# Kernel tuning notes

Hardware: AMD Instinct MI355X
Metric: run time of the kernel (lower is better)

Reference implementation:

```python
import jax, jax.numpy as jnp
import numpy as np

EPS = 1e-5
MAX_NORM = 1.0 - 1e-5  # clamp for atanh / ball projection


def mob_add(u, v):
    # Mobius addition on each d_ball (last dim), c=1
    uv = jnp.sum(u * v, axis=-1, keepdims=True)
    uu = jnp.sum(u * u, axis=-1, keepdims=True)
    vv = jnp.sum(v * v, axis=-1, keepdims=True)
    num = (1.0 + 2.0 * uv + vv) * u + (1.0 - uu) * v
    den = 1.0 + 2.0 * uv + uu * vv
    return num / jnp.maximum(den, EPS)


def log_map_zero(y):
    # log map at origin, per ball (last dim)
    n = jnp.linalg.norm(y, axis=-1, keepdims=True)
    n_c = jnp.clip(n, EPS, MAX_NORM)
    return jnp.arctanh(n_c) * y / n_c


def mob_mat_mul_d(W, x, d):
    # W: (n_in, d, n_out, d); x: (B, n_in, d) -> (B, n_out, d)
    # Mobius matvec on the flattened product-ball representation.
    B = x.shape[0]
    x_f = x.reshape(B, -1)                      # (B, n_in*d)
    W_f = W.reshape(x_f.shape[-1], -1)          # (n_in*d, n_out*d)
    Mx = x_f @ W_f                              # (B, n_out*d)
    x_n = jnp.clip(jnp.linalg.norm(x_f, axis=-1, keepdims=True), EPS, MAX_NORM)
    Mx_n = jnp.maximum(jnp.linalg.norm(Mx, axis=-1, keepdims=True), EPS)
    res = jnp.tanh(Mx_n / x_n * jnp.arctanh(x_n)) * (Mx / Mx_n)
    return res.reshape(B, -1, d)


def mob_pointwise_prod(x, u):
    # diagonal Mobius scaling of hyperbolic x by euclidean gate u, per ball
    ux = u * x
    x_n = jnp.clip(jnp.linalg.norm(x, axis=-1, keepdims=True), EPS, MAX_NORM)
    ux_n = jnp.maximum(jnp.linalg.norm(ux, axis=-1, keepdims=True), EPS)
    return jnp.tanh(ux_n / x_n * jnp.arctanh(x_n)) * (ux / ux_n)


def transition(W, h, U, x, b, d):
    Wh = mob_mat_mul_d(W, h, d)
    Ux = mob_mat_mul_d(U, x, d)
    return mob_add(mob_add(Wh, Ux), b)


def setup_inputs() -> dict:
    key = jax.random.key(0)
    ks = jax.random.split(key, 8)
    B, I, H, D = 16384, 256, 256, 4
    k = (1.0 / H) ** 0.5
    # scale points to lie strictly inside the Poincare ball
    hyp_x = 0.02 * jax.random.normal(ks[0], (B, I, D), dtype=jnp.float32)
    hidden = 0.02 * jax.random.normal(ks[1], (B, H, D), dtype=jnp.float32)
    mk = lambda kk, n_in: jax.random.uniform(kk, (n_in, D, H, D), minval=-k, maxval=k, dtype=jnp.float32)
    return dict(
        hyp_x=hyp_x, hidden=hidden,
        w_z=mk(ks[2], H), w_r=mk(ks[3], H), w_h=mk(ks[4], H),
        u_z=mk(ks[5], I), u_r=mk(ks[6], I), u_h=mk(ks[7], I),
        b_z=jnp.zeros((H, D), jnp.float32),
        b_r=jnp.zeros((H, D), jnp.float32),
        b_h=jnp.zeros((H, D), jnp.float32),
    )


def reference(hyp_x, hidden, w_z, w_r, w_h, u_z, u_r, u_h, b_z, b_r, b_h):
    d = hyp_x.shape[-1]
    z = jax.nn.sigmoid(log_map_zero(transition(w_z, hidden, u_z, hyp_x, b_z, d)))
    r = jax.nn.sigmoid(log_map_zero(transition(w_r, hidden, u_r, hyp_x, b_r, d)))
    r_point_h = mob_pointwise_prod(hidden, r)
    # NOTE: original code uses u_r here (not u_h) -- kept faithful
    h_tilde = transition(w_h, r_point_h, u_r, hyp_x, b_h, d)
    minus_h_oplus_htilde = mob_add(-hidden, h_tilde)
    new_h = mob_add(hidden, mob_pointwise_prod(minus_h_oplus_htilde, z))
    return new_h
```

## Files before the change

### kernel.cpp

```cpp
#include <hip/hip_runtime.h>
#include <stdint.h>

#define EPSF 1e-5f
#define MAXNF (1.0f - 1e-5f)

typedef __attribute__((ext_vector_type(8))) short short8;
typedef __attribute__((ext_vector_type(4))) float floatx4;

__device__ __forceinline__ unsigned short f2bf(float f){
  union { float f; uint32_t u; } v; v.f = f;
  return (unsigned short)((v.u + 0x7FFFu + ((v.u >> 16) & 1u)) >> 16);
}
__device__ __forceinline__ float bf_lo(uint32_t u){
  union { uint32_t u; float f; } v; v.u = u << 16; return v.f;
}
__device__ __forceinline__ float bf_hi(uint32_t u){
  union { uint32_t u; float f; } v; v.u = u & 0xffff0000u; return v.f;
}
__device__ __forceinline__ uint32_t cvtpk(float lo, float hi){
  uint32_t r; asm("v_cvt_pk_bf16_f32 %0, %1, %2" : "=v"(r) : "v"(lo), "v"(hi));
  return r;
}
__device__ __forceinline__ float fsqrt(float x){ return __builtin_amdgcn_sqrtf(x); }

__device__ __forceinline__ float4 ld_ball(const unsigned short* rowp, int b){
  const uint2 u = *(const uint2*)(rowp + 4*b);
  return make_float4(bf_lo(u.x), bf_hi(u.x), bf_lo(u.y), bf_hi(u.y));
}
__device__ __forceinline__ void st_ball(unsigned short* rowp, int b, float4 f){
  uint2 u; u.x = cvtpk(f.x, f.y); u.y = cvtpk(f.z, f.w);
  *(uint2*)(rowp + 4*b) = u;
}

__device__ __forceinline__ void gload16(const void* g, void* l){
  __builtin_amdgcn_global_load_lds(
      (__attribute__((address_space(1))) void*)(uintptr_t)g,
      (__attribute__((address_space(3))) void*)l, 16, 0, 0);
}

__device__ __forceinline__ float fatanh(float x){
  return 0.5f * __logf(__fdividef(1.f + x, 1.f - x));
}
__device__ __forceinline__ float ftanh_pos(float x){
  const float t = __expf(-2.f * x);
  return __fdividef(1.f - t, 1.f + t);
}
__device__ __forceinline__ float fsig(float x){
  return __fdividef(1.f, 1.f + __expf(-x));
}

__device__ __forceinline__ float wsum(float v){
  #pragma unroll
  for (int o = 32; o; o >>= 1) v += __shfl_xor(v, o);
  return v;
}

__device__ __forceinline__ float dot4(const float4 a, const float4 b){
  return a.x*b.x + a.y*b.y + a.z*b.z + a.w*b.w;
}
__device__ __forceinline__ float4 scal4(const float4 a, float s){
  return make_float4(a.x*s, a.y*s, a.z*s, a.w*s);
}
__device__ __forceinline__ float clipn(float n){ return fminf(fmaxf(n, EPSF), MAXNF); }

__device__ __forceinline__ float4 mob_add4(const float4 u, const float4 v){
  const float uv = dot4(u,v), uu = dot4(u,u), vv = dot4(v,v);
  const float cu = 1.f + 2.f*uv + vv, cv = 1.f - uu;
  const float inv = __fdividef(1.f, fmaxf(1.f + 2.f*uv + uu*vv, EPSF));
  return make_float4((cu*u.x + cv*v.x)*inv, (cu*u.y + cv*v.y)*inv,
                     (cu*u.z + cv*v.z)*inv, (cu*u.w + cv*v.w)*inv);
}
__device__ __forceinline__ float4 logmap_sig4(const float4 y){
  const float nc = clipn(fsqrt(dot4(y,y)));
  const float s = __fdividef(fatanh(nc), nc);
  return make_float4(fsig(s*y.x), fsig(s*y.y), fsig(s*y.z), fsig(s*y.w));
}
__device__ __forceinline__ float4 mob_pp4(const float4 x, const float4 u){
  const float4 ux = make_float4(u.x*x.x, u.y*x.y, u.z*x.z, u.w*x.w);
  const float xn = clipn(fsqrt(dot4(x,x)));
  const float uxn = fmaxf(fsqrt(dot4(ux,ux)), EPSF);
  const float s = __fdividef(ftanh_pos(__fdividef(uxn, xn) * fatanh(xn)), uxn);
  return scal4(ux, s);
}

__global__ void cast_norm_k(const float* __restrict__ X, unsigned short* __restrict__ Xbf,
                            float* __restrict__ nrm){
  const int lane = threadIdx.x & 63;
  const int row  = blockIdx.x*4 + (threadIdx.x >> 6);
  const float4* xr = (const float4*)(X + (size_t)row*1024);
  unsigned short* br_ = Xbf + (size_t)row*1024;
  float ss = 0.f;
  #pragma unroll
  for (int i = 0; i < 4; ++i){
    const int b = lane + 64*i;
    const float4 v = xr[b];
    st_ball(br_, b, v);
    ss += dot4(v, v);
  }
  ss = wsum(ss);
  if (lane == 0) nrm[row] = fsqrt(ss);
}

__global__ void wcast_k(const float* __restrict__ W, unsigned short* __restrict__ Wt){
  __shared__ float tile[32][33];
  const int tx = threadIdx.x, ty = threadIdx.y;
  const int k0 = blockIdx.x * 32, n0 = blockIdx.y * 32;
  #pragma unroll
  for (int i = 0; i < 4; ++i)
    tile[ty + i*8][tx] = W[(size_t)(k0 + ty + i*8) * 1024 + n0 + tx];
  __syncthreads();
  #pragma unroll
  for (int i = 0; i < 4; ++i)
    Wt[(size_t)(n0 + ty + i*8) * 1024 + k0 + tx] = f2bf(tile[tx][ty + i*8]);
}

#define NT 16

#define BARFENCE do { __builtin_amdgcn_s_barrier(); asm volatile("" ::: "memory"); } while(0)
#define LDA4(dst, MO) do { _Pragma("unroll") for (int m_=0;m_<4;++m_) \
  _Pragma("unroll") for (int k_=0;k_<2;++k_) \
    dst[m_][k_] = *(const short8*)(smem + bufb*32768 + abase + (MO+m_)*2048 + ((((k_<<2)+kg)^x7)<<4)); } while(0)
#define LDB2(dst, NO) do { _Pragma("unroll") for (int n_=0;n_<2;++n_) \
  _Pragma("unroll") for (int k_=0;k_<2;++k_) \
    dst[n_][k_] = *(const short8*)(smem + bufb*32768 + bbase + (NO+n_)*2048 + ((((k_<<2)+kg)^x7)<<4)); } while(0)
#define QUAD(AF, MO, BF, NO) do { _Pragma("unroll") for (int m_=0;m_<4;++m_) \
  _Pragma("unroll") for (int n_=0;n_<2;++n_) \
  _Pragma("unroll") for (int k_=0;k_<2;++k_) \
    acc[MO+m_][NO+n_] = __builtin_amdgcn_mfma_f32_16x16x32_bf16(AF[m_][k_], BF[n_][k_], acc[MO+m_][NO+n_], 0,0,0); } while(0)

__global__ __launch_bounds__(512, 2) void gemm8_k(const unsigned short* __restrict__ A,
                                                  const unsigned short* __restrict__ Bt,
                                                  unsigned short* __restrict__ C,
                                                  int lda, int ldc, int lnx){
  __shared__ unsigned char smem[131072];
  const int tid = threadIdx.x;
  const int lane = tid & 63, w = tid >> 6;
  const int wm = w >> 2, wn = w & 3;
  const int lr = lane & 15, kg = lane >> 4;
  const int x7 = lr & 7;

  const int wg  = blockIdx.x;
  const int xcd = wg & 7, q = wg >> 3;
  const int bx  = q & ((1 << lnx) - 1);
  const int by  = (xcd << 3) + (q >> lnx);
  const int row0 = by * 256, col0 = bx * 256;

  const int abase = (wm*128 + lr)*128;
  const int bbase = 65536 + (wn*64 + lr)*128;

  floatx4 acc[8][4] = {};

  auto stageH = [&](int regionByte, const unsigned short* src, int srow0, int ld, int kt){
    #pragma unroll
    for (int call = 0; call < 2; ++call){
      const int L  = (call << 9) + tid;
      const int rl = L >> 3;
      const int cc = (L & 7) ^ (rl & 7);
      gload16(src + (size_t)(srow0 + rl)*ld + kt*64 + cc*8,
              smem + regionByte + L*16);
    }
  };
  auto stageA = [&](int kt, int h){ stageH((kt&1)*32768 + h*16384, A, row0 + h*128, lda, kt); };
  auto stageB = [&](int kt, int h){ stageH(65536 + (kt&1)*32768 + h*16384, Bt, col0 + h*128, 1024, kt); };

  stageA(0,0); stageA(0,1); stageB(0,0); stageB(0,1);
  stageB(1,0); stageA(1,0); stageA(1,1);
  asm volatile("s_waitcnt vmcnt(6)" ::: "memory");
  __builtin_amdgcn_s_barrier();
  asm volatile("" ::: "memory");

  short8 aL[4][2], aH[4][2], bA[2][2], bB[2][2];

  for (int t = 0; t < NT; ++t){
    const int bufb = t & 1;
    LDA4(aL, 0); LDB2(bA, 0);
    if (t+1 < NT) stageB(t+1, 1);
    BARFENCE;
    __builtin_amdgcn_s_setprio(1); QUAD(aL, 0, bA, 0); __builtin_amdgcn_s_setprio(0);
    BARFENCE;
    LDB2(bB, 2);
    BARFENCE;
    __builtin_amdgcn_s_setprio(1); QUAD(aL, 0, bB, 2); __builtin_amdgcn_s_setprio(0);
    BARFENCE;
    LDA4(aH, 4);
    if (t+2 < NT) stageB(t+2, 0);
    BARFENCE;
    __builtin_amdgcn_s_setprio(1); QUAD(aH, 4, bB, 2); __builtin_amdgcn_s_setprio(0);
    BARFENCE;
    if (t+2 < NT){ stageA(t+2, 0); stageA(t+2, 1); }
    if (t+2 < NT)      asm volatile("s_waitcnt vmcnt(6)" ::: "memory");
    else if (t+1 < NT) asm volatile("s_waitcnt vmcnt(0)" ::: "memory");
    BARFENCE;
    __builtin_amdgcn_s_setprio(1); QUAD(aH, 4, bA, 0); __builtin_amdgcn_s_setprio(0);
    BARFENCE;
  }

  const int crow = row0 + wm*128;
  const int ccol = col0 + wn*64 + lr;
  #pragma unroll
  for (int m = 0; m < 8; ++m){
    #pragma unroll
    for (int j = 0; j < 4; ++j){
      unsigned short* cp = C + (size_t)(crow + m*16 + kg*4 + j)*ldc + ccol;
      #pragma unroll
      for (int n = 0; n < 4; ++n) cp[n*16] = f2bf(acc[m][n][j]);
    }
  }
}

__global__ __launch_bounds__(256) __attribute__((amdgpu_waves_per_eu(4,4)))
void epi1_k(unsigned short* C1, unsigned short* C2, const unsigned short* hbf,
            const float* bz, const float* br,
            const float* h_nrm, const float* x_nrm, float* rph_nrm){
  const int lane = threadIdx.x & 63;
  const int row  = blockIdx.x*4 + (threadIdx.x >> 6);
  unsigned short* c1lo = C1 + (size_t)row*2048;
  unsigned short* c1hi = c1lo + 1024;
  unsigned short* c2lo = C2 + (size_t)row*2048;
  unsigned short* c2hi = c2lo + 1024;
  const unsigned short* hr = hbf + (size_t)row*1024;

  float4 mzh[4], mrh[4], mzx[4], mrx[4];
  float s0 = 0.f, s1 = 0.f, s2 = 0.f, s3 = 0.f;
  #pragma unroll
  for (int i = 0; i < 4; ++i){
    const int b = lane + 64*i;
    mzh[i] = ld_ball(c1lo, b); mrh[i] = ld_ball(c1hi, b);
    mzx[i] = ld_ball(c2lo, b); mrx[i] = ld_ball(c2hi, b);
    s0 += dot4(mzh[i], mzh[i]); s1 += dot4(mzx[i], mzx[i]);
    s2 += dot4(mrh[i], mrh[i]); s3 += dot4(mrx[i], mrx[i]);
  }
  s0 = wsum(s0); s1 = wsum(s1); s2 = wsum(s2); s3 = wsum(s3);

  const float nMzh = fmaxf(fsqrt(s0), EPSF);
  const float nMzx = fmaxf(fsqrt(s1), EPSF);
  const float nMrh = fmaxf(fsqrt(s2), EPSF);
  const float nMrx = fmaxf(fsqrt(s3), EPSF);
  const float hnc = clipn(h_nrm[row]), xnc = clipn(x_nrm[row]);
  const float atH = fatanh(hnc), atX = fatanh(xnc);
  const float swz = __fdividef(ftanh_pos(__fdividef(nMzh, hnc)*atH), nMzh);
  const float suz = __fdividef(ftanh_pos(__fdividef(nMzx, xnc)*atX), nMzx);
  const float swr = __fdividef(ftanh_pos(__fdividef(nMrh, hnc)*atH), nMrh);
  const float sur = __fdividef(ftanh_pos(__fdividef(nMrx, xnc)*atX), nMrx);

  float sr = 0.f;
  #pragma unroll
  for (int i = 0; i < 4; ++i){
    const int b = lane + 64*i;
    const float4 bz4 = ((const float4*)bz)[b];
    const float4 br4 = ((const float4*)br)[b];
    const float4 z4  = logmap_sig4(mob_add4(mob_add4(scal4(mzh[i],swz), scal4(mzx[i],suz)), bz4));
    const float4 UxR = scal4(mrx[i], sur);
    const float4 r4  = logmap_sig4(mob_add4(mob_add4(scal4(mrh[i],swr), UxR), br4));
    st_ball(c1lo, b, z4);
    st_ball(c1hi, b, UxR);
    const float4 h4  = ld_ball(hr, b);
    const float4 rph = mob_pp4(h4, r4);
    st_ball(c2lo, b, rph);
    sr += dot4(rph, rph);
  }
  sr = wsum(sr);
  if (lane == 0) rph_nrm[row] = fsqrt(sr);
}

__global__ __launch_bounds__(256) __attribute__((amdgpu_waves_per_eu(4,4)))
void epi2_k(const unsigned short* C1, const unsigned short* C2,
            const unsigned short* hbf, const float* bh,
            const float* rph_nrm, float* out){
  const int lane = threadIdx.x & 63;
  const int row  = blockIdx.x*4 + (threadIdx.x >> 6);
  const unsigned short* c1lo = C1 + (size_t)row*2048;
  const unsigned short* c1hi = c1lo + 1024;
  const unsigned short* c2hi = C2 + (size_t)row*2048 + 1024;
  const unsigned short* hr = hbf + (size_t)row*1024;
  float4* outr = (float4*)(out + (size_t)row*1024);

  float4 mh[4];
  float ss = 0.f;
  #pragma unroll
  for (int i = 0; i < 4; ++i){
    mh[i] = ld_ball(c2hi, lane + 64*i);
    ss += dot4(mh[i], mh[i]);
  }
  ss = wsum(ss);
  const float nMh = fmaxf(fsqrt(ss), EPSF);
  const float rnc = clipn(rph_nrm[row]);
  const float swh = __fdividef(ftanh_pos(__fdividef(nMh, rnc)*fatanh(rnc)), nMh);

  #pragma unroll
  for (int i = 0; i < 4; ++i){
    const int b = lane + 64*i;
    const float4 WhH = scal4(mh[i], swh);
    const float4 Ux4 = ld_ball(c1hi, b);
    const float4 bh4 = ((const float4*)bh)[b];
    const float4 ht  = mob_add4(mob_add4(WhH, Ux4), bh4);
    const float4 h4  = ld_ball(hr, b);
    const float4 nh4 = make_float4(-h4.x, -h4.y, -h4.z, -h4.w);
    const float4 m4  = mob_add4(nh4, ht);
    const float4 z4  = ld_ball(c1lo, b);
    const float4 p4  = mob_pp4(m4, z4);
    outr[b] = mob_add4(h4, p4);
  }
}

extern "C" void kernel_launch(void* const* d_in, const int* in_sizes, int n_in,
                              void* d_out, int out_size, void* d_ws, size_t ws_size,
                              hipStream_t stream) {
  (void)in_sizes; (void)n_in; (void)out_size; (void)ws_size;
  const float* hyp_x  = (const float*)d_in[0];
  const float* hidden = (const float*)d_in[1];
  const float* w_z = (const float*)d_in[2];
  const float* w_r = (const float*)d_in[3];
  const float* w_h = (const float*)d_in[4];
  const float* u_z = (const float*)d_in[5];
  const float* u_r = (const float*)d_in[6];
  const float* b_z = (const float*)d_in[8];
  const float* b_r = (const float*)d_in[9];
  const float* b_h = (const float*)d_in[10];
  float* out = (float*)d_out;

  const size_t NROW = 16384, MAT = NROW*1024;
  unsigned short* hbf = (unsigned short*)d_ws;
  unsigned short* xbf = hbf + MAT;
  unsigned short* C1  = xbf + MAT;
  unsigned short* wzr = C1 + 2*MAT;
  unsigned short* uzr = wzr + 2*1048576;
  unsigned short* wht = uzr + 2*1048576;
  float* h_n   = (float*)(wht + 1048576);
  float* x_n   = h_n + NROW;
  float* rph_n = x_n + NROW;
  unsigned short* C2 = (unsigned short*)d_out;

  cast_norm_k<<<dim3(4096), dim3(256), 0, stream>>>(hidden, hbf, h_n);
  cast_norm_k<<<dim3(4096), dim3(256), 0, stream>>>(hyp_x, xbf, x_n);

  dim3 wg(32, 32), wb(32, 8);
  wcast_k<<<wg, wb, 0, stream>>>(w_z, wzr);
  wcast_k<<<wg, wb, 0, stream>>>(w_r, wzr + 1048576);
  wcast_k<<<wg, wb, 0, stream>>>(u_z, uzr);
  wcast_k<<<wg, wb, 0, stream>>>(u_r, uzr + 1048576);
  wcast_k<<<wg, wb, 0, stream>>>(w_h, wht);

  gemm8_k<<<dim3(512), dim3(512), 0, stream>>>(hbf, wzr, C1, 1024, 2048, 3);
  gemm8_k<<<dim3(512), dim3(512), 0, stream>>>(xbf, uzr, C2, 1024, 2048, 3);

  epi1_k<<<dim3(4096), dim3(256), 0, stream>>>(C1, C2, hbf, b_z, b_r, h_n, x_n, rph_n);

  gemm8_k<<<dim3(256), dim3(512), 0, stream>>>(C2, wht, C2 + 1024, 2048, 2048, 2);

  epi2_k<<<dim3(4096), dim3(256), 0, stream>>>(C1, C2, hbf, b_h, rph_n, out);
}
```

Measured before the change: 321.8 us.

## Prefetch next-tile LDS fragments and regroup global stages in GEMM main loop

Restructures the GEMM main loop schedule. The first A/B fragments for the next k-tile are now read from LDS at the end of the current iteration, overlapping the final MFMA quads. The B tile for t+2 is staged as a whole block mid-iteration, with the vmcnt waits and the prologue adjusted to match. The aim is to hide LDS read latency at the iteration boundary. The cost is tighter barrier and buffer-hazard reasoning, and possibly higher register pressure.

```diff
diff --git a/kernel.cpp b/kernel.cpp
--- a/kernel.cpp
+++ b/kernel.cpp
@@ -117,12 +117,12 @@
 #define NT 16
 
 #define BARFENCE do { __builtin_amdgcn_s_barrier(); asm volatile("" ::: "memory"); } while(0)
-#define LDA4(dst, MO) do { _Pragma("unroll") for (int m_=0;m_<4;++m_) \
+#define LDA4(dst, MO, BUF) do { _Pragma("unroll") for (int m_=0;m_<4;++m_) \
   _Pragma("unroll") for (int k_=0;k_<2;++k_) \
-    dst[m_][k_] = *(const short8*)(smem + bufb*32768 + abase + (MO+m_)*2048 + ((((k_<<2)+kg)^x7)<<4)); } while(0)
-#define LDB2(dst, NO) do { _Pragma("unroll") for (int n_=0;n_<2;++n_) \
+    dst[m_][k_] = *(const short8*)(smem + (BUF)*32768 + abase + (MO+m_)*2048 + ((((k_<<2)+kg)^x7)<<4)); } while(0)
+#define LDB2(dst, NO, BUF) do { _Pragma("unroll") for (int n_=0;n_<2;++n_) \
   _Pragma("unroll") for (int k_=0;k_<2;++k_) \
-    dst[n_][k_] = *(const short8*)(smem + bufb*32768 + bbase + (NO+n_)*2048 + ((((k_<<2)+kg)^x7)<<4)); } while(0)
+    dst[n_][k_] = *(const short8*)(smem + (BUF)*32768 + bbase + (NO+n_)*2048 + ((((k_<<2)+kg)^x7)<<4)); } while(0)
 #define QUAD(AF, MO, BF, NO) do { _Pragma("unroll") for (int m_=0;m_<4;++m_) \
   _Pragma("unroll") for (int n_=0;n_<2;++n_) \
   _Pragma("unroll") for (int k_=0;k_<2;++k_) \
@@ -164,34 +164,38 @@
   auto stageB = [&](int kt, int h){ stageH(65536 + (kt&1)*32768 + h*16384, Bt, col0 + h*128, 1024, kt); };
 
   stageA(0,0); stageA(0,1); stageB(0,0); stageB(0,1);
-  stageB(1,0); stageA(1,0); stageA(1,1);
-  asm volatile("s_waitcnt vmcnt(6)" ::: "memory");
-  __builtin_amdgcn_s_barrier();
-  asm volatile("" ::: "memory");
+  stageA(1,0); stageA(1,1); stageB(1,0); stageB(1,1);
+  asm volatile("s_waitcnt vmcnt(8)" ::: "memory");
+  BARFENCE;
 
   short8 aL[4][2], aH[4][2], bA[2][2], bB[2][2];
+  LDA4(aL, 0, 0);
+  LDB2(bA, 0, 0);
 
   for (int t = 0; t < NT; ++t){
     const int bufb = t & 1;
-    LDA4(aL, 0); LDB2(bA, 0);
-    if (t+1 < NT) stageB(t+1, 1);
+    LDB2(bB, 2, bufb);
     BARFENCE;
     __builtin_amdgcn_s_setprio(1); QUAD(aL, 0, bA, 0); __builtin_amdgcn_s_setprio(0);
     BARFENCE;
-    LDB2(bB, 2);
+    LDA4(aH, 4, bufb);
     BARFENCE;
     __builtin_amdgcn_s_setprio(1); QUAD(aL, 0, bB, 2); __builtin_amdgcn_s_setprio(0);
     BARFENCE;
-    LDA4(aH, 4);
-    if (t+2 < NT) stageB(t+2, 0);
+    if (t+2 < NT){
+      stageB(t+2,0); stageB(t+2,1);
+      asm volatile("s_waitcnt vmcnt(4)" ::: "memory");
+    } else if (t+1 < NT){
+      asm volatile("s_waitcnt vmcnt(0)" ::: "memory");
+    }
     BARFENCE;
     __builtin_amdgcn_s_setprio(1); QUAD(aH, 4, bB, 2); __builtin_amdgcn_s_setprio(0);
-    BARFENCE;
-    if (t+2 < NT){ stageA(t+2, 0); stageA(t+2, 1); }
-    if (t+2 < NT)      asm volatile("s_waitcnt vmcnt(6)" ::: "memory");
-    else if (t+1 < NT) asm volatile("s_waitcnt vmcnt(0)" ::: "memory");
+    if (t+1 < NT) LDA4(aL, 0, bufb^1);
+    BARFENCE;
+    if (t+2 < NT){ stageA(t+2,0); stageA(t+2,1); }
     BARFENCE;
     __builtin_amdgcn_s_setprio(1); QUAD(aH, 4, bA, 0); __builtin_amdgcn_s_setprio(0);
+    if (t+1 < NT) LDB2(bA, 0, bufb^1);
     BARFENCE;
   }
 
```

Result: no change. 324.0 us (+0.7%).
